# Performance work log

Hardware: AMD Instinct MI355X
Metric: run time of the kernel (lower is better)

## Reference

```python
import jax, jax.numpy as jnp
import numpy as np

N = 100_000   # nodes
E = 3_200_000 # edges (avg degree 32)
D = 256       # gnn width
H = 128       # mlp hidden
C = 5         # num classes


def _gcn_conv(x, W, b, src, dst, norm, n):
    # PyG GCNConv: h = x @ W^T, then symmetric-normalized scatter-add over edges
    h = x @ W.T
    msgs = norm[:, None] * h[src]                      # [E+N, out]
    out = jax.ops.segment_sum(msgs, dst, num_segments=n)
    return out + b


def setup_inputs() -> dict:
    key = jax.random.key(0)
    ks = jax.random.split(key, 8)
    x = jax.random.normal(ks[0], (N, D), dtype=jnp.float32)
    edge_index = jax.random.randint(ks[1], (2, E), 0, N, dtype=jnp.int32)
    def lin(k, out_d, in_d):
        return jax.random.normal(k, (out_d, in_d), dtype=jnp.float32) / np.sqrt(in_d).astype(np.float32)
    return {
        "x": x,
        "edge_index": edge_index,
        "W1": lin(ks[2], D, D), "b1": jnp.zeros((D,), jnp.float32),
        "W2": lin(ks[3], D, D), "b2": jnp.zeros((D,), jnp.float32),
        "Wm1": lin(ks[4], H, D), "bm1": jnp.zeros((H,), jnp.float32),
        "Wm2": lin(ks[5], C, H), "bm2": jnp.zeros((C,), jnp.float32),
    }


def reference(x, edge_index, W1, b1, W2, b2, Wm1, bm1, Wm2, bm2):
    # add self-loops (PyG GCNConv default add_self_loops=True)
    loop = jnp.arange(N, dtype=edge_index.dtype)
    src = jnp.concatenate([edge_index[0], loop])
    dst = jnp.concatenate([edge_index[1], loop])
    # symmetric normalization: deg from destination index (flow source_to_target)
    deg = jax.ops.segment_sum(jnp.ones(src.shape[0], x.dtype), dst, num_segments=N)
    dinv = jnp.where(deg > 0, jax.lax.rsqrt(deg), 0.0)
    norm = dinv[src] * dinv[dst]                       # [E+N]

    h = _gcn_conv(x, W1, b1, src, dst, norm, N)
    h = _gcn_conv(h, W2, b2, src, dst, norm, N)
    # MLP head (no activations in original module)
    h = h @ Wm1.T + bm1
    h = h @ Wm2.T + bm2
    return h
```

## Files before the change

### kernel.cpp

```cpp
#include <hip/hip_runtime.h>

#define N_NODES 100000
#define N_EDGES 3200000
#define DIM 256
#define HID 128
#define NCLS 5
#define BSH 8
#define BSZ 256
#define NBUCK 391
#define P1B 256
#define EPB 12500
#define HPKC 16

__global__ void k_zero(int* p, int n) {
    int i = blockIdx.x * 256 + threadIdx.x;
    if (i < n) p[i] = 0;
}

template<int K>
__global__ __launch_bounds__(256) void k_hp_stage(const float* __restrict__ A,
        const float* __restrict__ B, float* __restrict__ OUT)
{
    int t = threadIdx.x;
    int k0 = blockIdx.x * HPKC;
    float acc[NCLS] = {0, 0, 0, 0, 0};
    #pragma unroll
    for (int kk = 0; kk < HPKC; ++kk) {
        int k = k0 + kk;
        float b = B[k * DIM + t];
        #pragma unroll
        for (int c = 0; c < NCLS; ++c) acc[c] += A[c * K + k] * b;
    }
    #pragma unroll
    for (int c = 0; c < NCLS; ++c) unsafeAtomicAdd(&OUT[c * DIM + t], acc[c]);
}

__global__ __launch_bounds__(320) void k_hp_bias(const float* __restrict__ Wc,
        const float* __restrict__ W2c, const float* __restrict__ Wm2,
        const float* __restrict__ b1, const float* __restrict__ b2,
        const float* __restrict__ bm1, const float* __restrict__ bm2,
        float* __restrict__ bq, float* __restrict__ bc2)
{
    int c = threadIdx.x >> 6;
    int lane = threadIdx.x & 63;
    float s = 0.0f;
    for (int i = lane; i < DIM; i += 64) s += W2c[c * DIM + i] * b1[i];
    #pragma unroll
    for (int off = 32; off > 0; off >>= 1) s += __shfl_xor(s, off);
    float b = 0.0f;
    for (int k = lane; k < HID; k += 64) b += Wm2[c * HID + k] * bm1[k];
    for (int o = lane; o < DIM; o += 64) b += Wc[c * DIM + o] * b2[o];
    #pragma unroll
    for (int off = 32; off > 0; off >>= 1) b += __shfl_xor(b, off);
    if (lane == 0) { bq[c] = s; bc2[c] = bm2[c] + b; }
}

__global__ __launch_bounds__(1024) void k_p1hist(const int* __restrict__ dst,
        int* __restrict__ gcount, int* __restrict__ blockbase)
{
    __shared__ int lh[NBUCK];
    int tid = threadIdx.x;
    for (int i = tid; i < NBUCK; i += 1024) lh[i] = 0;
    __syncthreads();
    int s = blockIdx.x * EPB, e1 = s + EPB;
    for (int e = s + tid; e < e1; e += 1024) atomicAdd(&lh[dst[e] >> BSH], 1);
    __syncthreads();
    for (int i = tid; i < NBUCK; i += 1024) {
        int c = lh[i];
        blockbase[blockIdx.x * NBUCK + i] = c ? atomicAdd(&gcount[i], c) : 0;
    }
}
__global__ __launch_bounds__(512) void k_scanb(const int* __restrict__ gcount,
        int* __restrict__ gbase)
{
    __shared__ int sdata[512];
    int tid = threadIdx.x;
    int v = (tid < NBUCK) ? gcount[tid] : 0;
    sdata[tid] = v;
    __syncthreads();
    #pragma unroll
    for (int off = 1; off < 512; off <<= 1) {
        int t = (tid >= off) ? sdata[tid - off] : 0;
        __syncthreads();
        sdata[tid] += t;
        __syncthreads();
    }
    if (tid < NBUCK) gbase[tid] = sdata[tid] - v;
    if (tid == 0) gbase[NBUCK] = N_EDGES;
}
__global__ __launch_bounds__(1024) void k_p1scatter(const int* __restrict__ src,
        const int* __restrict__ dst, const int* __restrict__ gbase,
        const int* __restrict__ blockbase, unsigned* __restrict__ ebuf)
{
    __shared__ int lh[NBUCK];
    int tid = threadIdx.x;
    for (int i = tid; i < NBUCK; i += 1024) lh[i] = 0;
    __syncthreads();
    int s = blockIdx.x * EPB, e1 = s + EPB;
    for (int e = s + tid; e < e1; e += 1024) {
        int d = dst[e];
        int b = d >> BSH;
        int r = atomicAdd(&lh[b], 1);
        int pos = gbase[b] + blockbase[blockIdx.x * NBUCK + b] + r;
        ebuf[pos] = ((unsigned)src[e] << 8) | (unsigned)(d & 255);
    }
}
__global__ __launch_bounds__(512) void k_p2(const unsigned* __restrict__ ebuf,
        const int* __restrict__ gbase, int* __restrict__ rowptr,
        float* __restrict__ dinv, int* __restrict__ esrc)
{
    __shared__ int c[BSZ];
    __shared__ int sdata[BSZ];
    __shared__ int cur[BSZ];
    int tid = threadIdx.x, b = blockIdx.x;
    if (tid < BSZ) c[tid] = 0;
    __syncthreads();
    int s = gbase[b], e1 = gbase[b + 1];
    for (int e = s + tid; e < e1; e += 512) atomicAdd(&c[ebuf[e] & 255u], 1);
    __syncthreads();
    int cnt = (tid < BSZ) ? c[tid] : 0;
    if (tid < BSZ) sdata[tid] = cnt;
    __syncthreads();
    #pragma unroll
    for (int off = 1; off < BSZ; off <<= 1) {
        int t = (tid >= off && tid < BSZ) ? sdata[tid - off] : 0;
        __syncthreads();
        if (tid < BSZ) sdata[tid] += t;
        __syncthreads();
    }
    if (tid < BSZ) {
        int rp = s + sdata[tid] - cnt;
        cur[tid] = rp;
        int node = b * BSZ + tid;
        if (node < N_NODES) {
            rowptr[node] = rp;
            dinv[node] = rsqrtf((float)(cnt + 1));
        }
    }
    if (b == 0 && tid == 0) rowptr[N_NODES] = N_EDGES;
    __syncthreads();
    for (int e = s + tid; e < e1; e += 512) {
        unsigned p = ebuf[e];
        int pos = atomicAdd(&cur[p & 255u], 1);
        esrc[pos] = (int)(p >> 8);
    }
}

__global__ __launch_bounds__(256) void k_q(const float* __restrict__ x,
        const float* __restrict__ Wq, const float* __restrict__ dinv,
        float* __restrict__ qbuf)
{
    int wid = (blockIdx.x * 256 + threadIdx.x) >> 6;
    int lane = threadIdx.x & 63;
    int lane4 = lane * 4;
    int nwaves = gridDim.x * 4;
    float4 w[NCLS];
    #pragma unroll
    for (int c = 0; c < NCLS; ++c) w[c] = *(const float4*)(Wq + c * DIM + lane4);
    for (int d = wid; d < N_NODES; d += nwaves) {
        float4 xv = *(const float4*)(x + (size_t)d * DIM + lane4);
        float p[NCLS];
        #pragma unroll
        for (int c = 0; c < NCLS; ++c) {
            float s = xv.x * w[c].x + xv.y * w[c].y + xv.z * w[c].z + xv.w * w[c].w;
            #pragma unroll
            for (int off = 32; off > 0; off >>= 1) s += __shfl_xor(s, off);
            p[c] = s;
        }
        if (lane == 0) {
            float dv = dinv[d];
            #pragma unroll
            for (int c = 0; c < NCLS; ++c) qbuf[(size_t)d * 8 + c] = dv * p[c];
        }
    }
}

template<int MODE>
__global__ __launch_bounds__(256) void k_gather5(const float* __restrict__ in,
        const int* __restrict__ rowptr, const int* __restrict__ esrc,
        const float* __restrict__ dinv, const float* __restrict__ bias,
        float* __restrict__ out, int ostride)
{
    int gid = blockIdx.x * 256 + threadIdx.x;
    int d = gid >> 2, sub = gid & 3;
    if (d >= N_NODES) return;
    float acc0 = 0, acc1 = 0, acc2 = 0, acc3 = 0, acc4 = 0;
    int r0 = rowptr[d], r1 = rowptr[d + 1];
    for (int j = r0 + sub; j < r1; j += 4) {
        int s = esrc[j];
        float4 v = *(const float4*)(in + (size_t)s * 8);
        float v4 = in[(size_t)s * 8 + 4];
        acc0 += v.x; acc1 += v.y; acc2 += v.z; acc3 += v.w; acc4 += v4;
    }
    if (sub == 0) {
        float4 v = *(const float4*)(in + (size_t)d * 8);
        float v4 = in[(size_t)d * 8 + 4];
        acc0 += v.x; acc1 += v.y; acc2 += v.z; acc3 += v.w; acc4 += v4;
    }
    #pragma unroll
    for (int off = 1; off < 4; off <<= 1) {
        acc0 += __shfl_xor(acc0, off);
        acc1 += __shfl_xor(acc1, off);
        acc2 += __shfl_xor(acc2, off);
        acc3 += __shfl_xor(acc3, off);
        acc4 += __shfl_xor(acc4, off);
    }
    if (sub == 0) {
        float dv = dinv[d];
        float sc = (MODE == 1) ? dv * dv : dv;
        float bs = (MODE == 1) ? dv : 1.0f;
        out[(size_t)d * ostride + 0] = sc * acc0 + bs * bias[0];
        out[(size_t)d * ostride + 1] = sc * acc1 + bs * bias[1];
        out[(size_t)d * ostride + 2] = sc * acc2 + bs * bias[2];
        out[(size_t)d * ostride + 3] = sc * acc3 + bs * bias[3];
        out[(size_t)d * ostride + 4] = sc * acc4 + bs * bias[4];
    }
}

extern "C" void kernel_launch(void* const* d_in, const int* in_sizes, int n_in,
                              void* d_out, int out_size, void* d_ws, size_t ws_size,
                              hipStream_t stream)
{
    const float* x   = (const float*)d_in[0];
    const int*   ei  = (const int*)d_in[1];
    const float* W1  = (const float*)d_in[2];
    const float* b1  = (const float*)d_in[3];
    const float* W2  = (const float*)d_in[4];
    const float* b2  = (const float*)d_in[5];
    const float* Wm1 = (const float*)d_in[6];
    const float* bm1 = (const float*)d_in[7];
    const float* Wm2 = (const float*)d_in[8];
    const float* bm2 = (const float*)d_in[9];
    float* out = (float*)d_out;
    const int* src = ei;
    const int* dst = ei + N_EDGES;

    char* ws = (char*)d_ws;
    float* dinv     = (float*)   (ws + 0x0000000);
    int* rowptr     = (int*)     (ws + 0x0080000);
    int* esrc       = (int*)     (ws + 0x0200000);
    float* hpw      = (float*)   (ws + 0x0F00000);
    float* Wq       = hpw;
    float* Wc       = hpw + NCLS * DIM;
    float* W2c      = hpw + 2 * NCLS * DIM;
    int* gcount     = (int*)     (hpw + 3 * NCLS * DIM);
    float* bq       = (float*)   (ws + 0x0F10000);
    float* bc2      = (float*)   (ws + 0x0F11000);
    float* qbuf     = (float*)   (ws + 0x1000000);
    float* tbuf     = (float*)   (ws + 0x1400000);
    unsigned* ebuf  = (unsigned*)(ws + 0x1800000);
    int* blockbase  = (int*)     (ws + 0x2600000);
    int* gbase      = (int*)     (ws + 0x2700000);

    const int NZ = 3 * NCLS * DIM + NBUCK;
    k_zero<<<(NZ + 255) / 256, 256, 0, stream>>>((int*)hpw, NZ);

    k_hp_stage<HID><<<HID / HPKC, 256, 0, stream>>>(Wm2, Wm1, Wc);
    k_hp_stage<DIM><<<DIM / HPKC, 256, 0, stream>>>(Wc, W2, W2c);
    k_hp_bias<<<1, 320, 0, stream>>>(Wc, W2c, Wm2, b1, b2, bm1, bm2, bq, bc2);
    k_hp_stage<DIM><<<DIM / HPKC, 256, 0, stream>>>(W2c, W1, Wq);

    k_p1hist<<<P1B, 1024, 0, stream>>>(dst, gcount, blockbase);
    k_scanb<<<1, 512, 0, stream>>>(gcount, gbase);
    k_p1scatter<<<P1B, 1024, 0, stream>>>(src, dst, gbase, blockbase, ebuf);
    k_p2<<<NBUCK, 512, 0, stream>>>(ebuf, gbase, rowptr, dinv, esrc);

    k_q<<<2048, 256, 0, stream>>>(x, Wq, dinv, qbuf);

    const int GB = (N_NODES * 4 + 255) / 256;
    k_gather5<1><<<GB, 256, 0, stream>>>(qbuf, rowptr, esrc, dinv, bq, tbuf, 8);
    k_gather5<0><<<GB, 256, 0, stream>>>(tbuf, rowptr, esrc, dinv, bc2, out, NCLS);
}
```

Before: 330.9 us.

## Fuse histogram and scatter into one partition pass with fixed-capacity buckets

The separate histogram and scatter kernels are merged into one partition kernel. It keeps each thread's dst values and local ranks in registers, reserves bucket space with a global atomic, and writes into fixed-capacity per-bucket slots (CAP) instead of a prefix-scanned compact buffer. This removes one full pass over dst and the blockbase array, and the scan moves after partitioning so it only computes rowptr bases. The second pass now uses 1024 threads per block. The risk is bucket overflow if any 256-node bucket receives more than CAP edges, which holds for random uniform inputs but not for arbitrary graphs.

```diff
diff --git a/kernel.cpp b/kernel.cpp
--- a/kernel.cpp
+++ b/kernel.cpp
@@ -8,8 +8,10 @@
 #define BSH 8
 #define BSZ 256
 #define NBUCK 391
-#define P1B 256
-#define EPB 12500
+#define UNR 12
+#define EPB (UNR*1024)
+#define P1B 261
+#define CAP 10240
 #define HPKC 16
 
 __global__ void k_zero(int* p, int n) {
@@ -55,21 +57,40 @@
     if (lane == 0) { bq[c] = s; bc2[c] = bm2[c] + b; }
 }
 
-__global__ __launch_bounds__(1024) void k_p1hist(const int* __restrict__ dst,
-        int* __restrict__ gcount, int* __restrict__ blockbase)
+__global__ __launch_bounds__(1024) void k_part(const int* __restrict__ src,
+        const int* __restrict__ dst, int* __restrict__ gcur,
+        unsigned* __restrict__ ebuf)
 {
     __shared__ int lh[NBUCK];
+    __shared__ int bs[NBUCK];
     int tid = threadIdx.x;
     for (int i = tid; i < NBUCK; i += 1024) lh[i] = 0;
     __syncthreads();
-    int s = blockIdx.x * EPB, e1 = s + EPB;
-    for (int e = s + tid; e < e1; e += 1024) atomicAdd(&lh[dst[e] >> BSH], 1);
+    int e0 = blockIdx.x * EPB + tid;
+    int d[UNR], r[UNR];
+    #pragma unroll
+    for (int it = 0; it < UNR; ++it) {
+        int e = e0 + it * 1024;
+        d[it] = (e < N_EDGES) ? dst[e] : -1;
+        r[it] = (d[it] >= 0) ? atomicAdd(&lh[d[it] >> BSH], 1) : 0;
+    }
     __syncthreads();
     for (int i = tid; i < NBUCK; i += 1024) {
         int c = lh[i];
-        blockbase[blockIdx.x * NBUCK + i] = c ? atomicAdd(&gcount[i], c) : 0;
-    }
-}
+        bs[i] = c ? atomicAdd(&gcur[i], c) : 0;
+    }
+    __syncthreads();
+    #pragma unroll
+    for (int it = 0; it < UNR; ++it) {
+        int e = e0 + it * 1024;
+        if (d[it] >= 0) {
+            int b = d[it] >> BSH;
+            ebuf[(size_t)b * CAP + bs[b] + r[it]] =
+                ((unsigned)src[e] << 8) | (unsigned)(d[it] & 255);
+        }
+    }
+}
+
 __global__ __launch_bounds__(512) void k_scanb(const int* __restrict__ gcount,
         int* __restrict__ gbase)
 {
@@ -86,28 +107,11 @@
         __syncthreads();
     }
     if (tid < NBUCK) gbase[tid] = sdata[tid] - v;
-    if (tid == 0) gbase[NBUCK] = N_EDGES;
-}
-__global__ __launch_bounds__(1024) void k_p1scatter(const int* __restrict__ src,
-        const int* __restrict__ dst, const int* __restrict__ gbase,
-        const int* __restrict__ blockbase, unsigned* __restrict__ ebuf)
-{
-    __shared__ int lh[NBUCK];
-    int tid = threadIdx.x;
-    for (int i = tid; i < NBUCK; i += 1024) lh[i] = 0;
-    __syncthreads();
-    int s = blockIdx.x * EPB, e1 = s + EPB;
-    for (int e = s + tid; e < e1; e += 1024) {
-        int d = dst[e];
-        int b = d >> BSH;
-        int r = atomicAdd(&lh[b], 1);
-        int pos = gbase[b] + blockbase[blockIdx.x * NBUCK + b] + r;
-        ebuf[pos] = ((unsigned)src[e] << 8) | (unsigned)(d & 255);
-    }
-}
-__global__ __launch_bounds__(512) void k_p2(const unsigned* __restrict__ ebuf,
-        const int* __restrict__ gbase, int* __restrict__ rowptr,
-        float* __restrict__ dinv, int* __restrict__ esrc)
+}
+
+__global__ __launch_bounds__(1024) void k_p2(const unsigned* __restrict__ ebuf,
+        const int* __restrict__ gcount, const int* __restrict__ gbase,
+        int* __restrict__ rowptr, float* __restrict__ dinv, int* __restrict__ esrc)
 {
     __shared__ int c[BSZ];
     __shared__ int sdata[BSZ];
@@ -115,8 +119,9 @@
     int tid = threadIdx.x, b = blockIdx.x;
     if (tid < BSZ) c[tid] = 0;
     __syncthreads();
-    int s = gbase[b], e1 = gbase[b + 1];
-    for (int e = s + tid; e < e1; e += 512) atomicAdd(&c[ebuf[e] & 255u], 1);
+    const unsigned* eb = ebuf + (size_t)b * CAP;
+    int n = gcount[b];
+    for (int e = tid; e < n; e += 1024) atomicAdd(&c[eb[e] & 255u], 1);
     __syncthreads();
     int cnt = (tid < BSZ) ? c[tid] : 0;
     if (tid < BSZ) sdata[tid] = cnt;
@@ -129,7 +134,7 @@
         __syncthreads();
     }
     if (tid < BSZ) {
-        int rp = s + sdata[tid] - cnt;
+        int rp = gbase[b] + sdata[tid] - cnt;
         cur[tid] = rp;
         int node = b * BSZ + tid;
         if (node < N_NODES) {
@@ -139,8 +144,8 @@
     }
     if (b == 0 && tid == 0) rowptr[N_NODES] = N_EDGES;
     __syncthreads();
-    for (int e = s + tid; e < e1; e += 512) {
-        unsigned p = ebuf[e];
+    for (int e = tid; e < n; e += 1024) {
+        unsigned p = eb[e];
         int pos = atomicAdd(&cur[p & 255u], 1);
         esrc[pos] = (int)(p >> 8);
     }
@@ -243,14 +248,13 @@
     float* Wq       = hpw;
     float* Wc       = hpw + NCLS * DIM;
     float* W2c      = hpw + 2 * NCLS * DIM;
-    int* gcount     = (int*)     (hpw + 3 * NCLS * DIM);
+    int* gcur       = (int*)     (hpw + 3 * NCLS * DIM);
     float* bq       = (float*)   (ws + 0x0F10000);
     float* bc2      = (float*)   (ws + 0x0F11000);
     float* qbuf     = (float*)   (ws + 0x1000000);
     float* tbuf     = (float*)   (ws + 0x1400000);
     unsigned* ebuf  = (unsigned*)(ws + 0x1800000);
-    int* blockbase  = (int*)     (ws + 0x2600000);
-    int* gbase      = (int*)     (ws + 0x2700000);
+    int* gbase      = (int*)     (ws + 0x2800000);
 
     const int NZ = 3 * NCLS * DIM + NBUCK;
     k_zero<<<(NZ + 255) / 256, 256, 0, stream>>>((int*)hpw, NZ);
@@ -260,10 +264,9 @@
     k_hp_bias<<<1, 320, 0, stream>>>(Wc, W2c, Wm2, b1, b2, bm1, bm2, bq, bc2);
     k_hp_stage<DIM><<<DIM / HPKC, 256, 0, stream>>>(W2c, W1, Wq);
 
-    k_p1hist<<<P1B, 1024, 0, stream>>>(dst, gcount, blockbase);
-    k_scanb<<<1, 512, 0, stream>>>(gcount, gbase);
-    k_p1scatter<<<P1B, 1024, 0, stream>>>(src, dst, gbase, blockbase, ebuf);
-    k_p2<<<NBUCK, 512, 0, stream>>>(ebuf, gbase, rowptr, dinv, esrc);
+    k_part<<<P1B, 1024, 0, stream>>>(src, dst, gcur, ebuf);
+    k_scanb<<<1, 512, 0, stream>>>(gcur, gbase);
+    k_p2<<<NBUCK, 1024, 0, stream>>>(ebuf, gcur, gbase, rowptr, dinv, esrc);
 
     k_q<<<2048, 256, 0, stream>>>(x, Wq, dinv, qbuf);
 
```

Measured after the change: 347.3 us. 1.05x slower.

## Build CSR with global per-node atomics instead of two-pass bucketed radix sort

Applied to the files above, without the earlier changes.

Replaces the two-level bucket sort (block histograms, bucket scatter into a packed buffer, then a per-bucket local sort) with a simpler CSR build. It counts node degrees with global atomics, runs a hierarchical scan, and scatters sources using per-node atomic cursors. This drops the intermediate packed edge buffer and one full pass over the edges. The cost is 6.4M global atomics on random addresses, which are likely contended and uncoalesced.

```diff
diff --git a/kernel.cpp b/kernel.cpp
--- a/kernel.cpp
+++ b/kernel.cpp
@@ -5,11 +5,8 @@
 #define DIM 256
 #define HID 128
 #define NCLS 5
-#define BSH 8
 #define BSZ 256
 #define NBUCK 391
-#define P1B 256
-#define EPB 12500
 #define HPKC 16
 
 __global__ void k_zero(int* p, int n) {
@@ -55,27 +52,43 @@
     if (lane == 0) { bq[c] = s; bc2[c] = bm2[c] + b; }
 }
 
-__global__ __launch_bounds__(1024) void k_p1hist(const int* __restrict__ dst,
-        int* __restrict__ gcount, int* __restrict__ blockbase)
-{
-    __shared__ int lh[NBUCK];
-    int tid = threadIdx.x;
-    for (int i = tid; i < NBUCK; i += 1024) lh[i] = 0;
+__global__ __launch_bounds__(1024) void k_deg(const int* __restrict__ dst,
+        int* __restrict__ deg)
+{
+    int i = blockIdx.x * 1024 + threadIdx.x;
+    int stride = gridDim.x * 1024;
+    for (int e = i; e < N_EDGES; e += stride) atomicAdd(&deg[dst[e]], 1);
+}
+
+__global__ __launch_bounds__(256) void k_scanbuck(const int* __restrict__ deg,
+        int* __restrict__ rowptr, float* __restrict__ dinv, int* __restrict__ btot)
+{
+    __shared__ int sdata[BSZ];
+    int tid = threadIdx.x, b = blockIdx.x;
+    int node = b * BSZ + tid;
+    int v = (node < N_NODES) ? deg[node] : 0;
+    sdata[tid] = v;
     __syncthreads();
-    int s = blockIdx.x * EPB, e1 = s + EPB;
-    for (int e = s + tid; e < e1; e += 1024) atomicAdd(&lh[dst[e] >> BSH], 1);
-    __syncthreads();
-    for (int i = tid; i < NBUCK; i += 1024) {
-        int c = lh[i];
-        blockbase[blockIdx.x * NBUCK + i] = c ? atomicAdd(&gcount[i], c) : 0;
-    }
-}
-__global__ __launch_bounds__(512) void k_scanb(const int* __restrict__ gcount,
+    #pragma unroll
+    for (int off = 1; off < BSZ; off <<= 1) {
+        int t = (tid >= off) ? sdata[tid - off] : 0;
+        __syncthreads();
+        sdata[tid] += t;
+        __syncthreads();
+    }
+    if (node < N_NODES) {
+        rowptr[node] = sdata[tid] - v;
+        dinv[node] = rsqrtf((float)(v + 1));
+    }
+    if (tid == BSZ - 1) btot[b] = sdata[BSZ - 1];
+}
+
+__global__ __launch_bounds__(512) void k_scanb(const int* __restrict__ btot,
         int* __restrict__ gbase)
 {
     __shared__ int sdata[512];
     int tid = threadIdx.x;
-    int v = (tid < NBUCK) ? gcount[tid] : 0;
+    int v = (tid < NBUCK) ? btot[tid] : 0;
     sdata[tid] = v;
     __syncthreads();
     #pragma unroll
@@ -86,63 +99,29 @@
         __syncthreads();
     }
     if (tid < NBUCK) gbase[tid] = sdata[tid] - v;
-    if (tid == 0) gbase[NBUCK] = N_EDGES;
-}
-__global__ __launch_bounds__(1024) void k_p1scatter(const int* __restrict__ src,
-        const int* __restrict__ dst, const int* __restrict__ gbase,
-        const int* __restrict__ blockbase, unsigned* __restrict__ ebuf)
-{
-    __shared__ int lh[NBUCK];
-    int tid = threadIdx.x;
-    for (int i = tid; i < NBUCK; i += 1024) lh[i] = 0;
-    __syncthreads();
-    int s = blockIdx.x * EPB, e1 = s + EPB;
-    for (int e = s + tid; e < e1; e += 1024) {
-        int d = dst[e];
-        int b = d >> BSH;
-        int r = atomicAdd(&lh[b], 1);
-        int pos = gbase[b] + blockbase[blockIdx.x * NBUCK + b] + r;
-        ebuf[pos] = ((unsigned)src[e] << 8) | (unsigned)(d & 255);
-    }
-}
-__global__ __launch_bounds__(512) void k_p2(const unsigned* __restrict__ ebuf,
-        const int* __restrict__ gbase, int* __restrict__ rowptr,
-        float* __restrict__ dinv, int* __restrict__ esrc)
-{
-    __shared__ int c[BSZ];
-    __shared__ int sdata[BSZ];
-    __shared__ int cur[BSZ];
-    int tid = threadIdx.x, b = blockIdx.x;
-    if (tid < BSZ) c[tid] = 0;
-    __syncthreads();
-    int s = gbase[b], e1 = gbase[b + 1];
-    for (int e = s + tid; e < e1; e += 512) atomicAdd(&c[ebuf[e] & 255u], 1);
-    __syncthreads();
-    int cnt = (tid < BSZ) ? c[tid] : 0;
-    if (tid < BSZ) sdata[tid] = cnt;
-    __syncthreads();
-    #pragma unroll
-    for (int off = 1; off < BSZ; off <<= 1) {
-        int t = (tid >= off && tid < BSZ) ? sdata[tid - off] : 0;
-        __syncthreads();
-        if (tid < BSZ) sdata[tid] += t;
-        __syncthreads();
-    }
-    if (tid < BSZ) {
-        int rp = s + sdata[tid] - cnt;
-        cur[tid] = rp;
-        int node = b * BSZ + tid;
-        if (node < N_NODES) {
-            rowptr[node] = rp;
-            dinv[node] = rsqrtf((float)(cnt + 1));
-        }
+}
+
+__global__ __launch_bounds__(256) void k_fixup(const int* __restrict__ gbase,
+        int* __restrict__ rowptr, int* __restrict__ cur)
+{
+    int b = blockIdx.x, tid = threadIdx.x;
+    int node = b * BSZ + tid;
+    if (node < N_NODES) {
+        int rp = rowptr[node] + gbase[b];
+        rowptr[node] = rp;
+        cur[node] = rp;
     }
     if (b == 0 && tid == 0) rowptr[N_NODES] = N_EDGES;
-    __syncthreads();
-    for (int e = s + tid; e < e1; e += 512) {
-        unsigned p = ebuf[e];
-        int pos = atomicAdd(&cur[p & 255u], 1);
-        esrc[pos] = (int)(p >> 8);
+}
+
+__global__ __launch_bounds__(1024) void k_scat(const int* __restrict__ src,
+        const int* __restrict__ dst, int* __restrict__ cur, int* __restrict__ esrc)
+{
+    int i = blockIdx.x * 1024 + threadIdx.x;
+    int stride = gridDim.x * 1024;
+    for (int e = i; e < N_EDGES; e += stride) {
+        int pos = atomicAdd(&cur[dst[e]], 1);
+        esrc[pos] = src[e];
     }
 }
 
@@ -243,16 +222,16 @@
     float* Wq       = hpw;
     float* Wc       = hpw + NCLS * DIM;
     float* W2c      = hpw + 2 * NCLS * DIM;
-    int* gcount     = (int*)     (hpw + 3 * NCLS * DIM);
-    float* bq       = (float*)   (ws + 0x0F10000);
-    float* bc2      = (float*)   (ws + 0x0F11000);
-    float* qbuf     = (float*)   (ws + 0x1000000);
-    float* tbuf     = (float*)   (ws + 0x1400000);
-    unsigned* ebuf  = (unsigned*)(ws + 0x1800000);
-    int* blockbase  = (int*)     (ws + 0x2600000);
-    int* gbase      = (int*)     (ws + 0x2700000);
-
-    const int NZ = 3 * NCLS * DIM + NBUCK;
+    int* deg        = (int*)     (hpw + 3 * NCLS * DIM);
+    float* bq       = (float*)   (ws + 0x0FA0000);
+    float* bc2      = (float*)   (ws + 0x0FA1000);
+    int* btot       = (int*)     (ws + 0x0FB0000);
+    int* gbase      = (int*)     (ws + 0x0FB2000);
+    int* cur        = (int*)     (ws + 0x0FC0000);
+    float* qbuf     = (float*)   (ws + 0x1100000);
+    float* tbuf     = (float*)   (ws + 0x1500000);
+
+    const int NZ = 3 * NCLS * DIM + N_NODES;
     k_zero<<<(NZ + 255) / 256, 256, 0, stream>>>((int*)hpw, NZ);
 
     k_hp_stage<HID><<<HID / HPKC, 256, 0, stream>>>(Wm2, Wm1, Wc);
@@ -260,10 +239,11 @@
     k_hp_bias<<<1, 320, 0, stream>>>(Wc, W2c, Wm2, b1, b2, bm1, bm2, bq, bc2);
     k_hp_stage<DIM><<<DIM / HPKC, 256, 0, stream>>>(W2c, W1, Wq);
 
-    k_p1hist<<<P1B, 1024, 0, stream>>>(dst, gcount, blockbase);
-    k_scanb<<<1, 512, 0, stream>>>(gcount, gbase);
-    k_p1scatter<<<P1B, 1024, 0, stream>>>(src, dst, gbase, blockbase, ebuf);
-    k_p2<<<NBUCK, 512, 0, stream>>>(ebuf, gbase, rowptr, dinv, esrc);
+    k_deg<<<512, 1024, 0, stream>>>(dst, deg);
+    k_scanbuck<<<NBUCK, 256, 0, stream>>>(deg, rowptr, dinv, btot);
+    k_scanb<<<1, 512, 0, stream>>>(btot, gbase);
+    k_fixup<<<NBUCK, 256, 0, stream>>>(gbase, rowptr, cur);
+    k_scat<<<512, 1024, 0, stream>>>(src, dst, cur, esrc);
 
     k_q<<<2048, 256, 0, stream>>>(x, Wq, dinv, qbuf);
 
```

Measured after the change: 667.1 us. 2.02x slower.
